# Optimization experiments

Measured on AMD Instinct MI355X. Metric: run time of the kernel, lower is better.

## Reference

```python
import jax, jax.numpy as jnp
import numpy as np

N = 50000   # num_entities
E = 600000  # num_edges
D = 128     # dim
R = 200     # num_relations
T = 1000    # num_timestamps
L = 2       # num_layers


def setup_inputs() -> dict:
    key = jax.random.key(0)
    ks = jax.random.split(key, 16)
    edge_index = jax.random.randint(ks[0], (2, E), 0, N)
    edge_type = jax.random.randint(ks[1], (E,), 0, R)
    edge_time = jax.random.randint(ks[2], (E,), 0, T)
    edge_weight = jax.random.uniform(ks[3], (E,), dtype=jnp.float32)
    perm = jax.random.permutation(ks[4], N)
    entity_emb = jax.random.normal(ks[5], (N, D), dtype=jnp.float32)
    rel_emb = jax.random.normal(ks[6], (R, D), dtype=jnp.float32)
    time_emb = jax.random.normal(ks[7], (T, D), dtype=jnp.float32)
    s = 1.0 / np.sqrt(D)
    in_proj_w = jax.random.uniform(ks[8], (L, D, 2 * D), minval=-s, maxval=s)
    in_proj_b = jax.random.uniform(ks[9], (L, 2 * D), minval=-s, maxval=s)
    out_proj_w = jax.random.uniform(ks[10], (L, D, D), minval=-s, maxval=s)
    out_proj_b = jax.random.uniform(ks[11], (L, D), minval=-s, maxval=s)
    A = jax.random.normal(ks[12], (L, D)) * 0.1
    B = jax.random.normal(ks[13], (L, D)) * 0.1
    ln_g = jnp.ones((L, D), dtype=jnp.float32)
    ln_b = jnp.zeros((L, D), dtype=jnp.float32)
    return dict(edge_index=edge_index, edge_type=edge_type, edge_time=edge_time,
                edge_weight=edge_weight, perm=perm, entity_emb=entity_emb,
                rel_emb=rel_emb, time_emb=time_emb, in_proj_w=in_proj_w,
                in_proj_b=in_proj_b, out_proj_w=out_proj_w, out_proj_b=out_proj_b,
                A=A, B=B, ln_g=ln_g, ln_b=ln_b)


def _mamba_layer(x, Wi, bi, Wo, bo, A, B, g_ln, b_ln):
    # x: [N, D]
    zg = x @ Wi + bi                      # [N, 2D]
    z, g = jnp.split(zg, 2, axis=-1)
    g = jax.nn.sigmoid(g)

    def step(prev, zg_i):
        z_i, g_i = zg_i
        curr = g_i * (A * prev) + B * z_i
        return curr, curr

    _, h = jax.lax.scan(step, jnp.zeros((D,), x.dtype), (z, g))  # [N, D]
    y = x + h @ Wo + bo
    mu = jnp.mean(y, axis=-1, keepdims=True)
    var = jnp.mean((y - mu) ** 2, axis=-1, keepdims=True)
    return (y - mu) / jnp.sqrt(var + 1e-5) * g_ln + b_ln


def reference(edge_index, edge_type, edge_time, edge_weight, perm, entity_emb,
              rel_emb, time_emb, in_proj_w, in_proj_b, out_proj_w, out_proj_b,
              A, B, ln_g, ln_b):
    src, dst = edge_index[0], edge_index[1]
    msgs = entity_emb[src] + rel_emb[edge_type] + time_emb[edge_time]  # [E, D]
    sums = jax.ops.segment_sum(msgs * edge_weight[:, None], dst, num_segments=N)
    cnt = jax.ops.segment_sum(edge_weight, dst, num_segments=N)
    x = sums / jnp.maximum(cnt, 1.0)[:, None]          # scatter_mean
    x = x / jnp.maximum(jnp.linalg.norm(x, axis=1, keepdims=True), 1e-12)
    x = x[perm]
    for l in range(L):
        x = _mamba_layer(x, in_proj_w[l], in_proj_b[l], out_proj_w[l],
                         out_proj_b[l], A[l], B[l], ln_g[l], ln_b[l])
    return x
```

## Files before the change

### kernel.cpp

```cpp
#include <hip/hip_runtime.h>
#include <hip/hip_bf16.h>

typedef unsigned short ushort_t;
typedef unsigned int   uint_t;
typedef __attribute__((ext_vector_type(8))) short bf8;
typedef __attribute__((ext_vector_type(4))) float f32x4;

constexpr int N = 50000;
constexpr int E = 600000;
constexpr int D = 128;
constexpr int L = 2;
constexpr int NB = (N + 255) / 256;

constexpr int TR   = 48;
constexpr int LOOK = 16;
constexpr int RT   = TR + LOOK;
constexpr int NBLK = (N + TR - 1) / TR;
constexpr int SD   = 67;

__device__ __forceinline__ float us2f(ushort_t u) {
    union { uint_t i; float f; } c; c.i = (uint_t)u << 16; return c.f;
}
__device__ __forceinline__ ushort_t f2us(float f) {
    __hip_bfloat16 b = __float2bfloat16(f);
    return *(ushort_t*)&b;
}

__global__ __launch_bounds__(256) void k_hist(
    const int* __restrict__ dstp, int* __restrict__ hist)
{
    int e = blockIdx.x * 256 + threadIdx.x;
    if (e < E) atomicAdd(&hist[dstp[e]], 1);
}

__global__ __launch_bounds__(256) void k_scan1(
    const int* __restrict__ hist, int* __restrict__ part, int* __restrict__ bsum)
{
    int i = blockIdx.x * 256 + threadIdx.x;
    int v = (i < N) ? hist[i] : 0;
    int lane = threadIdx.x & 63, wv = threadIdx.x >> 6;
    int s = v;
    #pragma unroll
    for (int m = 1; m < 64; m <<= 1) {
        int t = __shfl_up(s, m, 64);
        if (lane >= m) s += t;
    }
    __shared__ int wsum[4];
    if (lane == 63) wsum[wv] = s;
    __syncthreads();
    int off = 0;
    for (int w = 0; w < wv; w++) off += wsum[w];
    if (i < N) part[i] = s - v + off;
    if (threadIdx.x == 255)
        bsum[blockIdx.x] = wsum[0] + wsum[1] + wsum[2] + wsum[3];
}

__global__ __launch_bounds__(256) void k_scan2(int* __restrict__ bsum)
{
    int i = threadIdx.x;
    int v = (i < NB) ? bsum[i] : 0;
    int lane = i & 63, wv = i >> 6;
    int s = v;
    #pragma unroll
    for (int m = 1; m < 64; m <<= 1) {
        int t = __shfl_up(s, m, 64);
        if (lane >= m) s += t;
    }
    __shared__ int wsum[4];
    if (lane == 63) wsum[wv] = s;
    __syncthreads();
    int off = 0;
    for (int w = 0; w < wv; w++) off += wsum[w];
    if (i < NB) bsum[i] = s - v + off;
}

__global__ __launch_bounds__(256) void k_finalize(
    const int* __restrict__ part, const int* __restrict__ bsum,
    int* __restrict__ cursor, int* __restrict__ rowst,
    const int* __restrict__ perm, int* __restrict__ invp)
{
    int i = blockIdx.x * 256 + threadIdx.x;
    if (i < N) {
        int b = part[i] + bsum[i >> 8];
        cursor[i] = b;
        rowst[i] = b;
        invp[perm[i]] = i;
    }
}

__global__ __launch_bounds__(256) void k_scatter(
    const int* __restrict__ eidx, const int* __restrict__ etype,
    const int* __restrict__ etime, const float* __restrict__ ew,
    int* __restrict__ cursor, int2* __restrict__ esort)
{
    int e = blockIdx.x * 256 + threadIdx.x;
    if (e >= E) return;
    int dst = eidx[E + e];
    int slot = atomicAdd(&cursor[dst], 1);
    int2 p;
    p.x = (eidx[e] & 0xffff) | (etype[e] << 16);
    p.y = (etime[e] & 0xffff) | ((int)f2us(ew[e]) << 16);
    esort[slot] = p;
}

__global__ __launch_bounds__(256) void k_ctab(
    const float* __restrict__ ent, const float* __restrict__ rel,
    const float* __restrict__ tim, ushort_t* __restrict__ entb,
    ushort_t* __restrict__ relb, ushort_t* __restrict__ timb)
{
    size_t t = (size_t)blockIdx.x * 256 + threadIdx.x;
    const float2* s; uint_t* d; size_t off;
    if (t < 3200000)        { s = (const float2*)ent; d = (uint_t*)entb; off = t; }
    else if (t < 3212800)   { s = (const float2*)rel; d = (uint_t*)relb; off = t - 3200000; }
    else if (t < 3276800)   { s = (const float2*)tim; d = (uint_t*)timb; off = t - 3212800; }
    else return;
    float2 v = s[off];
    d[off] = (uint_t)f2us(v.x) | ((uint_t)f2us(v.y) << 16);
}

__global__ __launch_bounds__(256) void k_castw(
    const float* __restrict__ Wi, const float* __restrict__ Wo,
    ushort_t* __restrict__ WiT, ushort_t* __restrict__ WoT)
{
    int t = blockIdx.x * 256 + threadIdx.x;
    if (t < L * 256 * 128) {
        int l = t / (256 * 128), r = t % (256 * 128);
        int n = r / 128, k = r % 128;
        WiT[t] = f2us(Wi[(size_t)l * 128 * 256 + k * 256 + n]);
    } else if (t < L * 256 * 128 + L * 128 * 128) {
        int u = t - L * 256 * 128;
        int l = u / (128 * 128), r = u % (128 * 128);
        int n = r / 128, k = r % 128;
        WoT[u] = f2us(Wo[(size_t)l * 128 * 128 + k * 128 + n]);
    }
}

__global__ __launch_bounds__(256) void k_agg(
    const int2* __restrict__ esort, const int* __restrict__ rowst,
    const int* __restrict__ hist, const int* __restrict__ invp,
    const ushort_t* __restrict__ entb, const ushort_t* __restrict__ relb,
    const ushort_t* __restrict__ timb, ushort_t* __restrict__ xbf)
{
    int wv = threadIdx.x >> 6, lane = threadIdx.x & 63;
    int d = blockIdx.x * 4 + wv;
    if (d >= N) return;
    int beg = rowst[d];
    int n = hist[d];

    float a0 = 0.f, a1 = 0.f, b0 = 0.f, b1 = 0.f, ws0 = 0.f, ws1 = 0.f;
    int j = 0;
    for (; j + 1 < n; j += 2) {
        int2 p = esort[beg + j];
        int2 q = esort[beg + j + 1];
        int  ps = p.x & 0xffff, pt = ((uint_t)p.x) >> 16;
        int  qs = q.x & 0xffff, qt = ((uint_t)q.x) >> 16;
        int  pm = p.y & 0xffff, qm = q.y & 0xffff;
        float wp = us2f((ushort_t)(((uint_t)p.y) >> 16));
        float wq = us2f((ushort_t)(((uint_t)q.y) >> 16));
        uint_t pa = *(const uint_t*)(entb + (size_t)ps * D + 2 * lane);
        uint_t qa = *(const uint_t*)(entb + (size_t)qs * D + 2 * lane);
        uint_t pb = *(const uint_t*)(relb + (size_t)pt * D + 2 * lane);
        uint_t qb = *(const uint_t*)(relb + (size_t)qt * D + 2 * lane);
        uint_t pc = *(const uint_t*)(timb + (size_t)pm * D + 2 * lane);
        uint_t qc = *(const uint_t*)(timb + (size_t)qm * D + 2 * lane);
        a0 += (us2f(pa & 0xffff) + us2f(pb & 0xffff) + us2f(pc & 0xffff)) * wp;
        a1 += (us2f(pa >> 16)    + us2f(pb >> 16)    + us2f(pc >> 16))    * wp;
        b0 += (us2f(qa & 0xffff) + us2f(qb & 0xffff) + us2f(qc & 0xffff)) * wq;
        b1 += (us2f(qa >> 16)    + us2f(qb >> 16)    + us2f(qc >> 16))    * wq;
        ws0 += wp; ws1 += wq;
    }
    if (j < n) {
        int2 p = esort[beg + j];
        int  ps = p.x & 0xffff, pt = ((uint_t)p.x) >> 16;
        int  pm = p.y & 0xffff;
        float wp = us2f((ushort_t)(((uint_t)p.y) >> 16));
        uint_t pa = *(const uint_t*)(entb + (size_t)ps * D + 2 * lane);
        uint_t pb = *(const uint_t*)(relb + (size_t)pt * D + 2 * lane);
        uint_t pc = *(const uint_t*)(timb + (size_t)pm * D + 2 * lane);
        a0 += (us2f(pa & 0xffff) + us2f(pb & 0xffff) + us2f(pc & 0xffff)) * wp;
        a1 += (us2f(pa >> 16)    + us2f(pb >> 16)    + us2f(pc >> 16))    * wp;
        ws0 += wp;
    }
    a0 += b0; a1 += b1;
    float inv = 1.0f / fmaxf(ws0 + ws1, 1.0f);
    a0 *= inv; a1 *= inv;

    float ss = a0 * a0 + a1 * a1;
    #pragma unroll
    for (int m = 32; m >= 1; m >>= 1) ss += __shfl_xor(ss, m, 64);
    float sc = 1.0f / fmaxf(sqrtf(ss), 1e-12f);

    int orow = invp[d];
    uint_t out = (uint_t)f2us(a0 * sc) | ((uint_t)f2us(a1 * sc) << 16);
    *(uint_t*)(xbf + (size_t)orow * D + 2 * lane) = out;
}

template <bool FINAL>
__global__ __launch_bounds__(256, 4) void k_layer(
    const ushort_t* __restrict__ xin, const ushort_t* __restrict__ WiT,
    const float* __restrict__ bi, const ushort_t* __restrict__ WoT,
    const float* __restrict__ bo, const float* __restrict__ Aw,
    const float* __restrict__ Bw, const float* __restrict__ lg,
    const float* __restrict__ lb, ushort_t* __restrict__ xoutb,
    float* __restrict__ outf)
{
    __shared__ uint_t zgp[128 * SD];
    ushort_t* zg16 = (ushort_t*)zgp;
    float*    redS = (float*)zgp;
    float*    redQ = redS + 192;
    float*    muA  = redS + 384;
    float*    rsA  = redS + 432;

    int tid = threadIdx.x;
    int w = tid >> 6, lane = tid & 63;
    int quad = lane >> 4, m = lane & 15;
    int r0 = blockIdx.x * TR;
    int base = r0 - LOOK;

    const bf8 zero8 = {0, 0, 0, 0, 0, 0, 0, 0};
    const f32x4 zero4 = {0.f, 0.f, 0.f, 0.f};

    {
        int cb = w * 64;
        #pragma unroll
        for (int sp = 0; sp < 2; sp++) {
            int c0 = cb + sp * 32 + m, c1 = c0 + 16;
            float bias0 = bi[c0], bias1 = bi[c1];
            bf8 b0[4], b1[4];
            #pragma unroll
            for (int kb = 0; kb < 4; kb++) {
                b0[kb] = *(const bf8*)(WiT + (size_t)c0 * 128 + kb * 32 + quad * 8);
                b1[kb] = *(const bf8*)(WiT + (size_t)c1 * 128 + kb * 32 + quad * 8);
            }
            #pragma unroll
            for (int rt = 0; rt < 4; rt++) {
                int gr = base + rt * 16 + m;
                bf8 a[4];
                if (gr >= 0 && gr < N) {
                    #pragma unroll
                    for (int kb = 0; kb < 4; kb++)
                        a[kb] = *(const bf8*)(xin + (size_t)gr * 128 + kb * 32 + quad * 8);
                } else {
                    #pragma unroll
                    for (int kb = 0; kb < 4; kb++) a[kb] = zero8;
                }
                f32x4 acc0 = zero4, acc1 = zero4;
                #pragma unroll
                for (int kb = 0; kb < 4; kb++) {
                    acc0 = __builtin_amdgcn_mfma_f32_16x16x32_bf16(a[kb], b0[kb], acc0, 0, 0, 0);
                    acc1 = __builtin_amdgcn_mfma_f32_16x16x32_bf16(a[kb], b1[kb], acc1, 0, 0, 0);
                }
                #pragma unroll
                for (int reg = 0; reg < 4; reg++) {
                    int rr = rt * 16 + quad * 4 + reg;
                    float v0 = acc0[reg] + bias0;
                    float v1 = acc1[reg] + bias1;
                    if (c0 < 128) {
                        zg16[(c0 * SD + rr) * 2] = f2us(v0);
                        zg16[(c1 * SD + rr) * 2] = f2us(v1);
                    } else {
                        zg16[((c0 - 128) * SD + rr) * 2 + 1] =
                            f2us(1.f / (1.f + __expf(-v0)));
                        zg16[((c1 - 128) * SD + rr) * 2 + 1] =
                            f2us(1.f / (1.f + __expf(-v1)));
                    }
                }
            }
        }
    }
    __syncthreads();

    if (tid < 128) {
        int d = tid;
        const uint_t* col = zgp + d * SD;
        ushort_t* hcol = (ushort_t*)col;
        float Ad = Aw[d], Bd = Bw[d], h = 0.f;
        if (base >= 0 && base + RT <= N) {
            #pragma unroll
            for (int b8 = 0; b8 < 8; b8++) {
                uint_t v[8];
                #pragma unroll
                for (int k = 0; k < 8; k++) v[k] = col[b8 * 8 + k];
                #pragma unroll
                for (int k = 0; k < 8; k++) {
                    int rr = b8 * 8 + k;
                    float z = us2f((ushort_t)(v[k] & 0xffff));
                    float g = us2f((ushort_t)(v[k] >> 16));
                    h = g * (Ad * h) + Bd * z;
                    if (rr >= LOOK) hcol[rr * 2] = f2us(h);
                }
            }
        } else {
            int s = (base < 0) ? LOOK : 0;
            int lim = N - base; if (lim > RT) lim = RT;
            for (int rr = s; rr < lim; rr++) {
                uint_t v = col[rr];
                float z = us2f((ushort_t)(v & 0xffff));
                float g = us2f((ushort_t)(v >> 16));
                h = g * (Ad * h) + Bd * z;
                if (rr >= LOOK) hcol[rr * 2] = f2us(h);
            }
        }
    }
    __syncthreads();

    float y[3][2][4];
    {
        int cb = w * 32;
        int c0 = cb + m, c1 = c0 + 16;
        float bias0 = bo[c0], bias1 = bo[c1];
        bf8 b0[4], b1[4];
        #pragma unroll
        for (int kb = 0; kb < 4; kb++) {
            b0[kb] = *(const bf8*)(WoT + (size_t)c0 * 128 + kb * 32 + quad * 8);
            b1[kb] = *(const bf8*)(WoT + (size_t)c1 * 128 + kb * 32 + quad * 8);
        }
        #pragma unroll
        for (int rt = 0; rt < 3; rt++) {
            int hrow = rt * 16 + m + LOOK;
            bf8 a[4];
            #pragma unroll
            for (int kb = 0; kb < 4; kb++) {
                #pragma unroll
                for (int j = 0; j < 8; j++)
                    a[kb][j] = (short)zg16[((kb * 32 + quad * 8 + j) * SD + hrow) * 2];
            }
            f32x4 acc0 = zero4, acc1 = zero4;
            #pragma unroll
            for (int kb = 0; kb < 4; kb++) {
                acc0 = __builtin_amdgcn_mfma_f32_16x16x32_bf16(a[kb], b0[kb], acc0, 0, 0, 0);
                acc1 = __builtin_amdgcn_mfma_f32_16x16x32_bf16(a[kb], b1[kb], acc1, 0, 0, 0);
            }
            #pragma unroll
            for (int reg = 0; reg < 4; reg++) {
                int gr = r0 + rt * 16 + quad * 4 + reg;
                float r0v = 0.f, r1v = 0.f;
                if (gr < N) {
                    r0v = us2f(xin[(size_t)gr * 128 + c0]);
                    r1v = us2f(xin[(size_t)gr * 128 + c1]);
                }
                y[rt][0][reg] = acc0[reg] + bias0 + r0v;
                y[rt][1][reg] = acc1[reg] + bias1 + r1v;
            }
        }
    }
    __syncthreads();

    {
        float ps[3][4], pq[3][4];
        #pragma unroll
        for (int rt = 0; rt < 3; rt++)
            #pragma unroll
            for (int reg = 0; reg < 4; reg++) {
                float v0 = y[rt][0][reg], v1 = y[rt][1][reg];
                float s = v0 + v1, q = v0 * v0 + v1 * v1;
                #pragma unroll
                for (int mk = 1; mk <= 8; mk <<= 1) {
                    s += __shfl_xor(s, mk, 64);
                    q += __shfl_xor(q, mk, 64);
                }
                ps[rt][reg] = s; pq[rt][reg] = q;
            }
        if (m == 0) {
            #pragma unroll
            for (int rt = 0; rt < 3; rt++)
                #pragma unroll
                for (int reg = 0; reg < 4; reg++) {
                    int row = rt * 16 + quad * 4 + reg;
                    redS[row * 4 + w] = ps[rt][reg];
                    redQ[row * 4 + w] = pq[rt][reg];
                }
        }
    }
    __syncthreads();
    if (tid < 48) {
        float s = redS[tid * 4] + redS[tid * 4 + 1] + redS[tid * 4 + 2] + redS[tid * 4 + 3];
        float q = redQ[tid * 4] + redQ[tid * 4 + 1] + redQ[tid * 4 + 2] + redQ[tid * 4 + 3];
        float mu = s * (1.f / 128.f);
        float var = q * (1.f / 128.f) - mu * mu;
        muA[tid] = mu;
        rsA[tid] = rsqrtf(var + 1e-5f);
    }
    __syncthreads();
    {
        int cb = w * 32;
        int c0 = cb + m, c1 = c0 + 16;
        float gl0 = lg[c0], gl1 = lg[c1], bl0 = lb[c0], bl1 = lb[c1];
        #pragma unroll
        for (int rt = 0; rt < 3; rt++)
            #pragma unroll
            for (int reg = 0; reg < 4; reg++) {
                int rr = rt * 16 + quad * 4 + reg;
                int gr = r0 + rr;
                if (gr < N) {
                    float mu = muA[rr], rs = rsA[rr];
                    float v0 = (y[rt][0][reg] - mu) * rs * gl0 + bl0;
                    float v1 = (y[rt][1][reg] - mu) * rs * gl1 + bl1;
                    if (FINAL) {
                        outf[(size_t)gr * 128 + c0] = v0;
                        outf[(size_t)gr * 128 + c1] = v1;
                    } else {
                        xoutb[(size_t)gr * 128 + c0] = f2us(v0);
                        xoutb[(size_t)gr * 128 + c1] = f2us(v1);
                    }
                }
            }
    }
}

extern "C" void kernel_launch(void* const* d_in, const int* in_sizes, int n_in,
                              void* d_out, int out_size, void* d_ws, size_t ws_size,
                              hipStream_t stream)
{
    const int*   eidx  = (const int*)d_in[0];
    const int*   etype = (const int*)d_in[1];
    const int*   etime = (const int*)d_in[2];
    const float* ew    = (const float*)d_in[3];
    const int*   perm  = (const int*)d_in[4];
    const float* ent   = (const float*)d_in[5];
    const float* rel   = (const float*)d_in[6];
    const float* tim   = (const float*)d_in[7];
    const float* Wi    = (const float*)d_in[8];
    const float* bi    = (const float*)d_in[9];
    const float* Wo    = (const float*)d_in[10];
    const float* bo    = (const float*)d_in[11];
    const float* Aw    = (const float*)d_in[12];
    const float* Bw    = (const float*)d_in[13];
    const float* lg    = (const float*)d_in[14];
    const float* lbp   = (const float*)d_in[15];

    char* base = (char*)d_ws;
    size_t o = 0;
    ushort_t* xbf  = (ushort_t*)(base + o); o += (size_t)N * D * 2;
    ushort_t* xb2  = (ushort_t*)(base + o); o += (size_t)N * D * 2;
    ushort_t* entb = (ushort_t*)(base + o); o += (size_t)N * D * 2;
    ushort_t* relb = (ushort_t*)(base + o); o += (size_t)200 * D * 2;
    ushort_t* timb = (ushort_t*)(base + o); o += (size_t)1000 * D * 2;
    ushort_t* WiT  = (ushort_t*)(base + o); o += (size_t)L * 256 * 128 * 2;
    ushort_t* WoT  = (ushort_t*)(base + o); o += (size_t)L * 128 * 128 * 2;
    int2*     esort  = (int2*)(base + o);   o += (size_t)E * 8;
    int*      hist   = (int*)(base + o);    o += (size_t)N * 4;
    int*      part   = (int*)(base + o);    o += (size_t)N * 4;
    int*      bsum   = (int*)(base + o);    o += 256 * 4;
    int*      cursor = (int*)(base + o);    o += (size_t)N * 4;
    int*      rowst  = (int*)(base + o);    o += (size_t)N * 4;
    int*      invp   = (int*)(base + o);    o += (size_t)N * 4;

    hipMemsetAsync(hist, 0, N * sizeof(int), stream);

    k_ctab    <<<12800, 256, 0, stream>>>(ent, rel, tim, entb, relb, timb);
    k_castw   <<<(L * 256 * 128 + L * 128 * 128 + 255) / 256, 256, 0, stream>>>(
                Wi, Wo, WiT, WoT);
    k_hist    <<<(E + 255) / 256, 256, 0, stream>>>(eidx + E, hist);
    k_scan1   <<<NB, 256, 0, stream>>>(hist, part, bsum);
    k_scan2   <<<1, 256, 0, stream>>>(bsum);
    k_finalize<<<NB, 256, 0, stream>>>(part, bsum, cursor, rowst, perm, invp);
    k_scatter <<<(E + 255) / 256, 256, 0, stream>>>(eidx, etype, etime, ew,
                                                    cursor, esort);
    k_agg     <<<(N + 3) / 4, 256, 0, stream>>>(esort, rowst, hist, invp,
                                                entb, relb, timb, xbf);

    k_layer<false><<<NBLK, 256, 0, stream>>>(
        xbf, WiT, bi, WoT, bo, Aw, Bw, lg, lbp, xb2, nullptr);
    k_layer<true><<<NBLK, 256, 0, stream>>>(
        xb2, WiT + (size_t)256 * 128, bi + 256, WoT + (size_t)128 * 128,
        bo + 128, Aw + 128, Bw + 128, lg + 128, lbp + 128,
        nullptr, (float*)d_out);
}
```

Measured before the change: 330.4 us.

## Compute Mamba scan in registers via parallel affine prefix over MFMA outputs

```diff
diff --git a/kernel.cpp b/kernel.cpp
--- a/kernel.cpp
+++ b/kernel.cpp
@@ -14,9 +14,8 @@
 
 constexpr int TR   = 48;
 constexpr int LOOK = 16;
-constexpr int RT   = TR + LOOK;
 constexpr int NBLK = (N + TR - 1) / TR;
-constexpr int SD   = 67;
+constexpr int HSTR = 136;
 
 __device__ __forceinline__ float us2f(ushort_t u) {
     union { uint_t i; float f; } c; c.i = (uint_t)u << 16; return c.f;
@@ -103,35 +102,33 @@
     esort[slot] = p;
 }
 
-__global__ __launch_bounds__(256) void k_ctab(
+__global__ __launch_bounds__(256) void k_cast(
     const float* __restrict__ ent, const float* __restrict__ rel,
-    const float* __restrict__ tim, ushort_t* __restrict__ entb,
-    ushort_t* __restrict__ relb, ushort_t* __restrict__ timb)
+    const float* __restrict__ tim, const float* __restrict__ Wi,
+    const float* __restrict__ Wo, ushort_t* __restrict__ entb,
+    ushort_t* __restrict__ relb, ushort_t* __restrict__ timb,
+    ushort_t* __restrict__ WiT, ushort_t* __restrict__ WoT)
 {
     size_t t = (size_t)blockIdx.x * 256 + threadIdx.x;
-    const float2* s; uint_t* d; size_t off;
-    if (t < 3200000)        { s = (const float2*)ent; d = (uint_t*)entb; off = t; }
-    else if (t < 3212800)   { s = (const float2*)rel; d = (uint_t*)relb; off = t - 3200000; }
-    else if (t < 3276800)   { s = (const float2*)tim; d = (uint_t*)timb; off = t - 3212800; }
-    else return;
-    float2 v = s[off];
-    d[off] = (uint_t)f2us(v.x) | ((uint_t)f2us(v.y) << 16);
-}
-
-__global__ __launch_bounds__(256) void k_castw(
-    const float* __restrict__ Wi, const float* __restrict__ Wo,
-    ushort_t* __restrict__ WiT, ushort_t* __restrict__ WoT)
-{
-    int t = blockIdx.x * 256 + threadIdx.x;
-    if (t < L * 256 * 128) {
-        int l = t / (256 * 128), r = t % (256 * 128);
-        int n = r / 128, k = r % 128;
-        WiT[t] = f2us(Wi[(size_t)l * 128 * 256 + k * 256 + n]);
-    } else if (t < L * 256 * 128 + L * 128 * 128) {
-        int u = t - L * 256 * 128;
-        int l = u / (128 * 128), r = u % (128 * 128);
-        int n = r / 128, k = r % 128;
-        WoT[u] = f2us(Wo[(size_t)l * 128 * 128 + k * 128 + n]);
+    if (t < 3276800) {
+        const float2* s; uint_t* d; size_t off;
+        if (t < 3200000)      { s = (const float2*)ent; d = (uint_t*)entb; off = t; }
+        else if (t < 3212800) { s = (const float2*)rel; d = (uint_t*)relb; off = t - 3200000; }
+        else                  { s = (const float2*)tim; d = (uint_t*)timb; off = t - 3212800; }
+        float2 v = s[off];
+        d[off] = (uint_t)f2us(v.x) | ((uint_t)f2us(v.y) << 16);
+    } else {
+        size_t u = t - 3276800;
+        if (u < (size_t)L * 256 * 128) {
+            int l = u / (256 * 128), r = u % (256 * 128);
+            int n = r / 128, k = r % 128;
+            WiT[u] = f2us(Wi[(size_t)l * 128 * 256 + k * 256 + n]);
+        } else if (u < (size_t)L * 256 * 128 + L * 128 * 128) {
+            size_t v = u - (size_t)L * 256 * 128;
+            int l = v / (128 * 128), r = v % (128 * 128);
+            int n = r / 128, k = r % 128;
+            WoT[v] = f2us(Wo[(size_t)l * 128 * 128 + k * 128 + n]);
+        }
     }
 }
 
@@ -147,42 +144,45 @@
     int beg = rowst[d];
     int n = hist[d];
 
-    float a0 = 0.f, a1 = 0.f, b0 = 0.f, b1 = 0.f, ws0 = 0.f, ws1 = 0.f;
+    float s0[4] = {0.f, 0.f, 0.f, 0.f};
+    float s1[4] = {0.f, 0.f, 0.f, 0.f};
+    float sw[4] = {0.f, 0.f, 0.f, 0.f};
+
     int j = 0;
-    for (; j + 1 < n; j += 2) {
+    for (; j + 3 < n; j += 4) {
+        int2 rec[4];
+        #pragma unroll
+        for (int u = 0; u < 4; u++) rec[u] = esort[beg + j + u];
+        #pragma unroll
+        for (int u = 0; u < 4; u++) {
+            int  sA = rec[u].x & 0xffff, tA = ((uint_t)rec[u].x) >> 16;
+            int  mA = rec[u].y & 0xffff;
+            float w = us2f((ushort_t)(((uint_t)rec[u].y) >> 16));
+            uint_t va = *(const uint_t*)(entb + (size_t)sA * D + 2 * lane);
+            uint_t vb = *(const uint_t*)(relb + (size_t)tA * D + 2 * lane);
+            uint_t vc = *(const uint_t*)(timb + (size_t)mA * D + 2 * lane);
+            s0[u] += (us2f(va & 0xffff) + us2f(vb & 0xffff) + us2f(vc & 0xffff)) * w;
+            s1[u] += (us2f(va >> 16)    + us2f(vb >> 16)    + us2f(vc >> 16))    * w;
+            sw[u] += w;
+        }
+    }
+    for (; j < n; j++) {
         int2 p = esort[beg + j];
-        int2 q = esort[beg + j + 1];
-        int  ps = p.x & 0xffff, pt = ((uint_t)p.x) >> 16;
-        int  qs = q.x & 0xffff, qt = ((uint_t)q.x) >> 16;
-        int  pm = p.y & 0xffff, qm = q.y & 0xffff;
-        float wp = us2f((ushort_t)(((uint_t)p.y) >> 16));
-        float wq = us2f((ushort_t)(((uint_t)q.y) >> 16));
-        uint_t pa = *(const uint_t*)(entb + (size_t)ps * D + 2 * lane);
-        uint_t qa = *(const uint_t*)(entb + (size_t)qs * D + 2 * lane);
-        uint_t pb = *(const uint_t*)(relb + (size_t)pt * D + 2 * lane);
-        uint_t qb = *(const uint_t*)(relb + (size_t)qt * D + 2 * lane);
-        uint_t pc = *(const uint_t*)(timb + (size_t)pm * D + 2 * lane);
-        uint_t qc = *(const uint_t*)(timb + (size_t)qm * D + 2 * lane);
-        a0 += (us2f(pa & 0xffff) + us2f(pb & 0xffff) + us2f(pc & 0xffff)) * wp;
-        a1 += (us2f(pa >> 16)    + us2f(pb >> 16)    + us2f(pc >> 16))    * wp;
-        b0 += (us2f(qa & 0xffff) + us2f(qb & 0xffff) + us2f(qc & 0xffff)) * wq;
-        b1 += (us2f(qa >> 16)    + us2f(qb >> 16)    + us2f(qc >> 16))    * wq;
-        ws0 += wp; ws1 += wq;
-    }
-    if (j < n) {
-        int2 p = esort[beg + j];
-        int  ps = p.x & 0xffff, pt = ((uint_t)p.x) >> 16;
-        int  pm = p.y & 0xffff;
-        float wp = us2f((ushort_t)(((uint_t)p.y) >> 16));
-        uint_t pa = *(const uint_t*)(entb + (size_t)ps * D + 2 * lane);
-        uint_t pb = *(const uint_t*)(relb + (size_t)pt * D + 2 * lane);
-        uint_t pc = *(const uint_t*)(timb + (size_t)pm * D + 2 * lane);
-        a0 += (us2f(pa & 0xffff) + us2f(pb & 0xffff) + us2f(pc & 0xffff)) * wp;
-        a1 += (us2f(pa >> 16)    + us2f(pb >> 16)    + us2f(pc >> 16))    * wp;
-        ws0 += wp;
-    }
-    a0 += b0; a1 += b1;
-    float inv = 1.0f / fmaxf(ws0 + ws1, 1.0f);
+        int  sA = p.x & 0xffff, tA = ((uint_t)p.x) >> 16;
+        int  mA = p.y & 0xffff;
+        float w = us2f((ushort_t)(((uint_t)p.y) >> 16));
+        uint_t va = *(const uint_t*)(entb + (size_t)sA * D + 2 * lane);
+        uint_t vb = *(const uint_t*)(relb + (size_t)tA * D + 2 * lane);
+        uint_t vc = *(const uint_t*)(timb + (size_t)mA * D + 2 * lane);
+        s0[0] += (us2f(va & 0xffff) + us2f(vb & 0xffff) + us2f(vc & 0xffff)) * w;
+        s1[0] += (us2f(va >> 16)    + us2f(vb >> 16)    + us2f(vc >> 16))    * w;
+        sw[0] += w;
+    }
+    float a0 = (s0[0] + s0[1]) + (s0[2] + s0[3]);
+    float a1 = (s1[0] + s1[1]) + (s1[2] + s1[3]);
+    float wsum = (sw[0] + sw[1]) + (sw[2] + sw[3]);
+
+    float inv = 1.0f / fmaxf(wsum, 1.0f);
     a0 *= inv; a1 *= inv;
 
     float ss = a0 * a0 + a1 * a1;
@@ -204,12 +204,8 @@
     const float* __restrict__ lb, ushort_t* __restrict__ xoutb,
     float* __restrict__ outf)
 {
-    __shared__ uint_t zgp[128 * SD];
-    ushort_t* zg16 = (ushort_t*)zgp;
-    float*    redS = (float*)zgp;
-    float*    redQ = redS + 192;
-    float*    muA  = redS + 384;
-    float*    rsA  = redS + 432;
+    __shared__ ushort_t hs[TR * HSTR];
+    __shared__ float redS[TR * 4], redQ[TR * 4], muA[TR], rsA[TR];
 
     int tid = threadIdx.x;
     int w = tid >> 6, lane = tid & 63;
@@ -220,85 +216,88 @@
     const bf8 zero8 = {0, 0, 0, 0, 0, 0, 0, 0};
     const f32x4 zero4 = {0.f, 0.f, 0.f, 0.f};
 
+    int cz0 = w * 32 + m;
+    int cz1 = cz0 + 16;
+
+    float Ad0 = Aw[cz0], Bd0 = Bw[cz0];
+    float Ad1 = Aw[cz1], Bd1 = Bw[cz1];
+    float bz0 = bi[cz0], bz1 = bi[cz1];
+    float bg0 = bi[cz0 + 128], bg1 = bi[cz1 + 128];
+
+    bf8 Bz0[4], Bz1[4], Bg0[4], Bg1[4];
     {
-        int cb = w * 64;
-        #pragma unroll
-        for (int sp = 0; sp < 2; sp++) {
-            int c0 = cb + sp * 32 + m, c1 = c0 + 16;
-            float bias0 = bi[c0], bias1 = bi[c1];
-            bf8 b0[4], b1[4];
-            #pragma unroll
-            for (int kb = 0; kb < 4; kb++) {
-                b0[kb] = *(const bf8*)(WiT + (size_t)c0 * 128 + kb * 32 + quad * 8);
-                b1[kb] = *(const bf8*)(WiT + (size_t)c1 * 128 + kb * 32 + quad * 8);
-            }
-            #pragma unroll
-            for (int rt = 0; rt < 4; rt++) {
-                int gr = base + rt * 16 + m;
-                bf8 a[4];
-                if (gr >= 0 && gr < N) {
-                    #pragma unroll
-                    for (int kb = 0; kb < 4; kb++)
-                        a[kb] = *(const bf8*)(xin + (size_t)gr * 128 + kb * 32 + quad * 8);
-                } else {
-                    #pragma unroll
-                    for (int kb = 0; kb < 4; kb++) a[kb] = zero8;
-                }
-                f32x4 acc0 = zero4, acc1 = zero4;
-                #pragma unroll
-                for (int kb = 0; kb < 4; kb++) {
-                    acc0 = __builtin_amdgcn_mfma_f32_16x16x32_bf16(a[kb], b0[kb], acc0, 0, 0, 0);
-                    acc1 = __builtin_amdgcn_mfma_f32_16x16x32_bf16(a[kb], b1[kb], acc1, 0, 0, 0);
-                }
-                #pragma unroll
-                for (int reg = 0; reg < 4; reg++) {
-                    int rr = rt * 16 + quad * 4 + reg;
-                    float v0 = acc0[reg] + bias0;
-                    float v1 = acc1[reg] + bias1;
-                    if (c0 < 128) {
-                        zg16[(c0 * SD + rr) * 2] = f2us(v0);
-                        zg16[(c1 * SD + rr) * 2] = f2us(v1);
-                    } else {
-                        zg16[((c0 - 128) * SD + rr) * 2 + 1] =
-                            f2us(1.f / (1.f + __expf(-v0)));
-                        zg16[((c1 - 128) * SD + rr) * 2 + 1] =
-                            f2us(1.f / (1.f + __expf(-v1)));
-                    }
-                }
-            }
-        }
-    }
-    __syncthreads();
-
-    if (tid < 128) {
-        int d = tid;
-        const uint_t* col = zgp + d * SD;
-        ushort_t* hcol = (ushort_t*)col;
-        float Ad = Aw[d], Bd = Bw[d], h = 0.f;
-        if (base >= 0 && base + RT <= N) {
-            #pragma unroll
-            for (int b8 = 0; b8 < 8; b8++) {
-                uint_t v[8];
-                #pragma unroll
-                for (int k = 0; k < 8; k++) v[k] = col[b8 * 8 + k];
-                #pragma unroll
-                for (int k = 0; k < 8; k++) {
-                    int rr = b8 * 8 + k;
-                    float z = us2f((ushort_t)(v[k] & 0xffff));
-                    float g = us2f((ushort_t)(v[k] >> 16));
-                    h = g * (Ad * h) + Bd * z;
-                    if (rr >= LOOK) hcol[rr * 2] = f2us(h);
-                }
-            }
+        int colz0 = w * 32 + m, colz1 = colz0 + 16;
+        #pragma unroll
+        for (int kb = 0; kb < 4; kb++) {
+            int ko = kb * 32 + quad * 8;
+            Bz0[kb] = *(const bf8*)(WiT + (size_t)colz0 * 128 + ko);
+            Bz1[kb] = *(const bf8*)(WiT + (size_t)colz1 * 128 + ko);
+            Bg0[kb] = *(const bf8*)(WiT + (size_t)(colz0 + 128) * 128 + ko);
+            Bg1[kb] = *(const bf8*)(WiT + (size_t)(colz1 + 128) * 128 + ko);
+        }
+    }
+
+    float carry0 = 0.f, carry1 = 0.f;
+    for (int rt = 0; rt < 4; rt++) {
+        int gr = base + rt * 16 + m;
+        bf8 a[4];
+        if (gr >= 0 && gr < N) {
+            #pragma unroll
+            for (int kb = 0; kb < 4; kb++)
+                a[kb] = *(const bf8*)(xin + (size_t)gr * 128 + kb * 32 + quad * 8);
         } else {
-            int s = (base < 0) ? LOOK : 0;
-            int lim = N - base; if (lim > RT) lim = RT;
-            for (int rr = s; rr < lim; rr++) {
-                uint_t v = col[rr];
-                float z = us2f((ushort_t)(v & 0xffff));
-                float g = us2f((ushort_t)(v >> 16));
-                h = g * (Ad * h) + Bd * z;
-                if (rr >= LOOK) hcol[rr * 2] = f2us(h);
+            #pragma unroll
+            for (int kb = 0; kb < 4; kb++) a[kb] = zero8;
+        }
+        f32x4 az0 = zero4, az1 = zero4, ag0 = zero4, ag1 = zero4;
+        #pragma unroll
+        for (int kb = 0; kb < 4; kb++) {
+            az0 = __builtin_amdgcn_mfma_f32_16x16x32_bf16(a[kb], Bz0[kb], az0, 0, 0, 0);
+            az1 = __builtin_amdgcn_mfma_f32_16x16x32_bf16(a[kb], Bz1[kb], az1, 0, 0, 0);
+            ag0 = __builtin_amdgcn_mfma_f32_16x16x32_bf16(a[kb], Bg0[kb], ag0, 0, 0, 0);
+            ag1 = __builtin_amdgcn_mfma_f32_16x16x32_bf16(a[kb], Bg1[kb], ag1, 0, 0, 0);
+        }
+        float P0 = 1.f, Q0 = 0.f, P1 = 1.f, Q1 = 0.f;
+        #pragma unroll
+        for (int reg = 0; reg < 4; reg++) {
+            int grr = base + rt * 16 + quad * 4 + reg;
+            bool ok = (grr >= 0) && (grr < N);
+            float z0 = az0[reg] + bz0, z1 = az1[reg] + bz1;
+            float g0 = 1.f / (1.f + __expf(-(ag0[reg] + bg0)));
+            float g1 = 1.f / (1.f + __expf(-(ag1[reg] + bg1)));
+            float ca0 = ok ? g0 * Ad0 : 0.f, cb0 = ok ? Bd0 * z0 : 0.f;
+            float ca1 = ok ? g1 * Ad1 : 0.f, cb1 = ok ? Bd1 * z1 : 0.f;
+            az0[reg] = ca0; ag0[reg] = cb0;
+            az1[reg] = ca1; ag1[reg] = cb1;
+            P0 = ca0 * P0; Q0 = ca0 * Q0 + cb0;
+            P1 = ca1 * P1; Q1 = ca1 * Q1 + cb1;
+        }
+        float Pp, Qp;
+        Pp = __shfl_up(P0, 16, 64); Qp = __shfl_up(Q0, 16, 64);
+        if (quad >= 1) { Q0 = P0 * Qp + Q0; P0 = P0 * Pp; }
+        Pp = __shfl_up(P1, 16, 64); Qp = __shfl_up(Q1, 16, 64);
+        if (quad >= 1) { Q1 = P1 * Qp + Q1; P1 = P1 * Pp; }
+        Pp = __shfl_up(P0, 32, 64); Qp = __shfl_up(Q0, 32, 64);
+        if (quad >= 2) { Q0 = P0 * Qp + Q0; P0 = P0 * Pp; }
+        Pp = __shfl_up(P1, 32, 64); Qp = __shfl_up(Q1, 32, 64);
+        if (quad >= 2) { Q1 = P1 * Qp + Q1; P1 = P1 * Pp; }
+        float Pe0 = __shfl_up(P0, 16, 64), Qe0 = __shfl_up(Q0, 16, 64);
+        float Pe1 = __shfl_up(P1, 16, 64), Qe1 = __shfl_up(Q1, 16, 64);
+        if (quad == 0) { Pe0 = 1.f; Qe0 = 0.f; Pe1 = 1.f; Qe1 = 0.f; }
+        float h0 = Pe0 * carry0 + Qe0;
+        float h1 = Pe1 * carry1 + Qe1;
+        float Pc0 = __shfl(P0, m + 48, 64), Qc0 = __shfl(Q0, m + 48, 64);
+        float Pc1 = __shfl(P1, m + 48, 64), Qc1 = __shfl(Q1, m + 48, 64);
+        carry0 = Pc0 * carry0 + Qc0;
+        carry1 = Pc1 * carry1 + Qc1;
+        #pragma unroll
+        for (int reg = 0; reg < 4; reg++) {
+            h0 = az0[reg] * h0 + ag0[reg];
+            h1 = az1[reg] * h1 + ag1[reg];
+            if (rt >= 1) {
+                int lrow = (rt - 1) * 16 + quad * 4 + reg;
+                hs[lrow * HSTR + cz0] = f2us(h0);
+                hs[lrow * HSTR + cz1] = f2us(h1);
             }
         }
     }
@@ -306,25 +305,21 @@
 
     float y[3][2][4];
     {
-        int cb = w * 32;
-        int c0 = cb + m, c1 = c0 + 16;
+        int c0 = w * 32 + m, c1 = c0 + 16;
         float bias0 = bo[c0], bias1 = bo[c1];
         bf8 b0[4], b1[4];
         #pragma unroll
         for (int kb = 0; kb < 4; kb++) {
-            b0[kb] = *(const bf8*)(WoT + (size_t)c0 * 128 + kb * 32 + quad * 8);
-            b1[kb] = *(const bf8*)(WoT + (size_t)c1 * 128 + kb * 32 + quad * 8);
+            int ko = kb * 32 + quad * 8;
+            b0[kb] = *(const bf8*)(WoT + (size_t)c0 * 128 + ko);
+            b1[kb] = *(const bf8*)(WoT + (size_t)c1 * 128 + ko);
         }
         #pragma unroll
         for (int rt = 0; rt < 3; rt++) {
-            int hrow = rt * 16 + m + LOOK;
             bf8 a[4];
             #pragma unroll
-            for (int kb = 0; kb < 4; kb++) {
-                #pragma unroll
-                for (int j = 0; j < 8; j++)
-                    a[kb][j] = (short)zg16[((kb * 32 + quad * 8 + j) * SD + hrow) * 2];
-            }
+            for (int kb = 0; kb < 4; kb++)
+                a[kb] = *(const bf8*)(hs + (rt * 16 + m) * HSTR + kb * 32 + quad * 8);
             f32x4 acc0 = zero4, acc1 = zero4;
             #pragma unroll
             for (int kb = 0; kb < 4; kb++) {
@@ -344,10 +339,8 @@
             }
         }
     }
-    __syncthreads();
 
     {
-        float ps[3][4], pq[3][4];
         #pragma unroll
         for (int rt = 0; rt < 3; rt++)
             #pragma unroll
@@ -359,21 +352,15 @@
                     s += __shfl_xor(s, mk, 64);
                     q += __shfl_xor(q, mk, 64);
                 }
-                ps[rt][reg] = s; pq[rt][reg] = q;
+                if (m == 0) {
+                    int row = rt * 16 + quad * 4 + reg;
+                    redS[row * 4 + w] = s;
+                    redQ[row * 4 + w] = q;
+                }
             }
-        if (m == 0) {
-            #pragma unroll
-            for (int rt = 0; rt < 3; rt++)
-                #pragma unroll
-                for (int reg = 0; reg < 4; reg++) {
-                    int row = rt * 16 + quad * 4 + reg;
-                    redS[row * 4 + w] = ps[rt][reg];
-                    redQ[row * 4 + w] = pq[rt][reg];
-                }
-        }
     }
     __syncthreads();
-    if (tid < 48) {
+    if (tid < TR) {
         float s = redS[tid * 4] + redS[tid * 4 + 1] + redS[tid * 4 + 2] + redS[tid * 4 + 3];
         float q = redQ[tid * 4] + redQ[tid * 4 + 1] + redQ[tid * 4 + 2] + redQ[tid * 4 + 3];
         float mu = s * (1.f / 128.f);
@@ -383,8 +370,7 @@
     }
     __syncthreads();
     {
-        int cb = w * 32;
-        int c0 = cb + m, c1 = c0 + 16;
+        int c0 = w * 32 + m, c1 = c0 + 16;
         float gl0 = lg[c0], gl1 = lg[c1], bl0 = lb[c0], bl1 = lb[c1];
         #pragma unroll
         for (int rt = 0; rt < 3; rt++)
@@ -448,9 +434,8 @@
 
     hipMemsetAsync(hist, 0, N * sizeof(int), stream);
 
-    k_ctab    <<<12800, 256, 0, stream>>>(ent, rel, tim, entb, relb, timb);
-    k_castw   <<<(L * 256 * 128 + L * 128 * 128 + 255) / 256, 256, 0, stream>>>(
-                Wi, Wo, WiT, WoT);
+    k_cast    <<<13185, 256, 0, stream>>>(ent, rel, tim, Wi, Wo,
+                                          entb, relb, timb, WiT, WoT);
     k_hist    <<<(E + 255) / 256, 256, 0, stream>>>(eidx + E, hist);
     k_scan1   <<<NB, 256, 0, stream>>>(hist, part, bsum);
     k_scan2   <<<1, 256, 0, stream>>>(bsum);
```

New measurement: 303.6 us. 1.09x faster.
